# Kernel optimization log

Hardware: AMD Instinct MI355X
Metric: run time of the kernel (lower is better)

## Reference

```python
import jax, jax.numpy as jnp
import numpy as np

B, H, Wd, C = 8, 64, 64, 128
KH, KW = 3, 3
N = KH * KW  # kernel_n
F = 256


def _grid_offset(h, w, kh, kw):
    """Replicates the TensorLayer grid construction exactly, including the
    (2,kh,kw)->(kh*kw,2) reshape of the stacked meshgrid."""
    n = kh * kw
    initial = np.stack(np.meshgrid(np.arange(kh), np.arange(kw), indexing='ij'))  # (2,kh,kw)
    initial = initial.reshape(-1, 2).astype(np.float32)  # (n,2), faithful flattening order
    gy = np.arange(-int((kh - 1) / 2.0), h - int((kh - 1) / 2.0))
    gx = np.arange(-int((kw - 1) / 2.0), w - int((kw - 1) / 2.0))
    grid = np.stack(np.meshgrid(gy, gx, indexing='ij'), axis=-1).astype(np.float32)  # (h,w,2)
    grid = np.tile(grid[:, :, None, :], (1, 1, n, 1))  # (h,w,n,2)
    return jnp.asarray(grid + initial[None, None, :, :])  # (h,w,n,2)


def setup_inputs() -> dict:
    key = jax.random.key(0)
    k1, k2, k3 = jax.random.split(key, 3)
    x = jax.random.normal(k1, (B, H, Wd, C), dtype=jnp.float32)
    offsets = jax.random.normal(k2, (B, H, Wd, 2 * N), dtype=jnp.float32)
    W = jax.random.normal(k3, (N, C, F), dtype=jnp.float32) * 0.02  # truncated_normal(0.02) analogue
    b = jnp.zeros((F,), dtype=jnp.float32)
    return {"x": x, "offsets": offsets, "W": W, "b": b}


def reference(x, offsets, W, b):
    h, w = x.shape[1], x.shape[2]
    grid = _grid_offset(h, w, KH, KW)  # (h,w,n,2)
    coords = grid[None] + offsets.reshape(x.shape[0], h, w, N, 2)  # (b,h,w,n,2)
    cy = jnp.clip(coords[..., 0], 0.0, jnp.float32(h - 1))
    cx = jnp.clip(coords[..., 1], 0.0, jnp.float32(w - 1))
    y0 = jnp.floor(cy).astype(jnp.int32)
    y1 = jnp.ceil(cy).astype(jnp.int32)
    x0 = jnp.floor(cx).astype(jnp.int32)
    x1 = jnp.ceil(cx).astype(jnp.int32)

    bidx = jnp.arange(x.shape[0])[:, None, None, None]

    def gather(yy, xx):
        return x[bidx, yy, xx]  # (b,h,w,n,c)

    v_lt = gather(y0, x0)
    v_rb = gather(y1, x1)
    v_lb = gather(y0, x1)  # (lt_y, rb_x) as in original
    v_rt = gather(y1, x0)  # (rb_y, lt_x) as in original

    fy = (cy - y0.astype(cy.dtype))[..., None]
    fx = (cx - x0.astype(cx.dtype))[..., None]
    vals_t = v_lt + (v_rt - v_lt) * fy
    vals_b = v_lb + (v_rb - v_lb) * fy
    mapped = vals_t + (vals_b - vals_t) * fx  # (b,h,w,n,c)

    # conv3d with kernel [1,1,n,c,f] + VALID == contraction over (n,c)
    out = jnp.einsum('bhwnc,ncf->bhwf', mapped, W) + b
    return out
```

## Files before the change

kernel.cpp:

```cpp
#include <hip/hip_runtime.h>

#define HH 64
#define WW 64
#define CC 128
#define FF 256
#define NTAP 9
#define KD 1152
#define MTOT 32768
#define XELEMS (8 * HH * WW * CC)
#define XCVT_BLOCKS (XELEMS / (256 * 8))
#define WT_BLOCKS 144

typedef __attribute__((ext_vector_type(8))) short bf16x8;
typedef __attribute__((ext_vector_type(4))) float floatx4;

__device__ __constant__ int c_iy[9] = {0,0,1,2,2,1,0,2,1};
__device__ __constant__ int c_ix[9] = {0,1,1,2,0,2,1,0,2};

__device__ inline unsigned short f2bf(float v) {
  union { float f; unsigned u; } c; c.f = v;
  unsigned r = (c.u + 0x7FFFu + ((c.u >> 16) & 1u)) >> 16;
  return (unsigned short)r;
}
__device__ inline float bflo(unsigned u) {
  union { unsigned u; float f; } c; c.u = u << 16; return c.f;
}
__device__ inline float bfhi(unsigned u) {
  union { unsigned u; float f; } c; c.u = u & 0xFFFF0000u; return c.f;
}

__global__ void prep_kernel(const float* __restrict__ X, const float* __restrict__ W,
                            unsigned short* __restrict__ Xb, unsigned short* __restrict__ Wt) {
  const int blk = blockIdx.x;
  if (blk < XCVT_BLOCKS) {
    const int t = blk * 256 + threadIdx.x;
    const float4* src = (const float4*)(X + (size_t)t * 8);
    float4 a = src[0], b2 = src[1];
    bf16x8 o;
    o[0] = (short)f2bf(a.x);  o[1] = (short)f2bf(a.y);
    o[2] = (short)f2bf(a.z);  o[3] = (short)f2bf(a.w);
    o[4] = (short)f2bf(b2.x); o[5] = (short)f2bf(b2.y);
    o[6] = (short)f2bf(b2.z); o[7] = (short)f2bf(b2.w);
    *(bf16x8*)(Xb + (size_t)t * 8) = o;
  } else {
    const int t = (blk - XCVT_BLOCKS) * 256 + threadIdx.x;
    const int f = t & 255;
    const int k0 = (t >> 8) * 8;
    unsigned short o[8];
#pragma unroll
    for (int i2 = 0; i2 < 8; ++i2)
      o[i2] = f2bf(W[(size_t)(k0 + i2) * FF + f]);
    *(uint4*)(Wt + (size_t)f * KD + k0) = *(uint4*)o;
  }
}

__global__ __launch_bounds__(256, 4) void interp_kernel(
    const unsigned short* __restrict__ Xb, const float* __restrict__ Off,
    unsigned short* __restrict__ Mp)
{
  const int blk = blockIdx.x;
  const int b   = blk & 7;
  const int pg  = blk >> 3;
  const int tid = threadIdx.x;
  const int g   = tid >> 4;
  const int c   = tid & 15;
  const int pos_local = pg * 16 + g;
  const int y = pos_local >> 6;
  const int x = pos_local & 63;

  const unsigned short* xb = Xb + (size_t)b * (HH * WW * CC);
  const float* offp = Off + ((size_t)(b * HH + y) * WW + x) * (2 * NTAP);
  unsigned short* dstrow = Mp + (size_t)(b * 4096 + pos_local) * KD + c * 8;

#pragma unroll
  for (int n = 0; n < NTAP; ++n) {
    float2 off2 = *(const float2*)(offp + 2 * n);
    float cy = (float)(y - 1 + c_iy[n]) + off2.x;
    float cx = (float)(x - 1 + c_ix[n]) + off2.y;
    cy = fminf(fmaxf(cy, 0.f), 63.f);
    cx = fminf(fmaxf(cx, 0.f), 63.f);
    float fy0 = floorf(cy), fy1 = ceilf(cy);
    float fx0 = floorf(cx), fx1 = ceilf(cx);
    int y0 = (int)fy0, y1 = (int)fy1, x0 = (int)fx0, x1 = (int)fx1;
    float fy = cy - fy0;
    float fx = cx - fx0;

    const uint4 q00 = *(const uint4*)(xb + (y0 * WW + x0) * CC + c * 8);
    const uint4 q10 = *(const uint4*)(xb + (y1 * WW + x0) * CC + c * 8);
    const uint4 q01 = *(const uint4*)(xb + (y0 * WW + x1) * CC + c * 8);
    const uint4 q11 = *(const uint4*)(xb + (y1 * WW + x1) * CC + c * 8);

    const unsigned u00[4] = {q00.x, q00.y, q00.z, q00.w};
    const unsigned u10[4] = {q10.x, q10.y, q10.z, q10.w};
    const unsigned u01[4] = {q01.x, q01.y, q01.z, q01.w};
    const unsigned u11[4] = {q11.x, q11.y, q11.z, q11.w};

    unsigned outw[4];
#pragma unroll
    for (int j = 0; j < 4; ++j) {
      float v00 = bflo(u00[j]), v10 = bflo(u10[j]), v01 = bflo(u01[j]), v11 = bflo(u11[j]);
      float tx = v00 + (v10 - v00) * fy;
      float tb = v01 + (v11 - v01) * fy;
      unsigned short rlo = f2bf(tx + (tb - tx) * fx);
      v00 = bfhi(u00[j]); v10 = bfhi(u10[j]); v01 = bfhi(u01[j]); v11 = bfhi(u11[j]);
      tx = v00 + (v10 - v00) * fy;
      tb = v01 + (v11 - v01) * fy;
      unsigned short rhi = f2bf(tx + (tb - tx) * fx);
      outw[j] = (unsigned)rlo | ((unsigned)rhi << 16);
    }
    *(uint4*)(dstrow + n * CC) = make_uint4(outw[0], outw[1], outw[2], outw[3]);
  }
}

__global__ __launch_bounds__(256, 4) void gemm_kernel(
    const unsigned short* __restrict__ Mp, const unsigned short* __restrict__ Wt,
    const float* __restrict__ bias, float* __restrict__ Out)
{
  __shared__ unsigned short smA[64 * 64];
  __shared__ unsigned short smB[128 * 64];

  const int blk = blockIdx.x;
  const int b   = blk & 7;
  const int q   = blk >> 3;
  const int fb  = q & 1;
  const int i   = q >> 1;
  const int m0  = b * 4096 + i * 64;
  const int f0  = fb * 128;
  const int tid = threadIdx.x;
  const int wave = tid >> 6, lane = tid & 63;
  const int wm = (wave & 1) * 32;
  const int wf = (wave >> 1) * 64;
  const int arow = lane & 15, aq = lane >> 4;
  const int srow = tid >> 3;
  const int sch  = tid & 7;

  floatx4 acc[2][4];
#pragma unroll
  for (int mt = 0; mt < 2; ++mt)
#pragma unroll
    for (int ft = 0; ft < 4; ++ft)
      acc[mt][ft] = (floatx4){0.f, 0.f, 0.f, 0.f};

#define STAGE(KT)                                                                    \
  {                                                                                  \
    _Pragma("unroll")                                                                \
    for (int p = 0; p < 2; ++p) {                                                    \
      int row = p * 32 + srow;                                                       \
      int chp = sch ^ (row & 7);                                                     \
      const unsigned short* gp = Mp + (size_t)(m0 + row) * KD + (KT) * 64 + chp * 8; \
      unsigned short* l = (unsigned short*)&smA[row * 64 + sch * 8];                 \
      __builtin_amdgcn_global_load_lds(                                              \
          (const __attribute__((address_space(1))) unsigned int*)gp,                 \
          (__attribute__((address_space(3))) unsigned int*)l, 16, 0, 0);             \
    }                                                                                \
    _Pragma("unroll")                                                                \
    for (int p = 0; p < 4; ++p) {                                                    \
      int row = p * 32 + srow;                                                       \
      int chp = sch ^ (row & 7);                                                     \
      const unsigned short* gp = Wt + (size_t)(f0 + row) * KD + (KT) * 64 + chp * 8; \
      unsigned short* l = (unsigned short*)&smB[row * 64 + sch * 8];                 \
      __builtin_amdgcn_global_load_lds(                                              \
          (const __attribute__((address_space(1))) unsigned int*)gp,                 \
          (__attribute__((address_space(3))) unsigned int*)l, 16, 0, 0);             \
    }                                                                                \
  }

  STAGE(0)
  __syncthreads();

  for (int kt = 0; kt < 18; ++kt) {
#pragma unroll
    for (int ks = 0; ks < 2; ++ks) {
      bf16x8 afr[2], bfr[4];
      const int slot = (((ks * 4 + aq) ^ (arow & 7)) * 8);
#pragma unroll
      for (int mt = 0; mt < 2; ++mt)
        afr[mt] = *(const bf16x8*)&smA[(wm + mt * 16 + arow) * 64 + slot];
#pragma unroll
      for (int ft = 0; ft < 4; ++ft)
        bfr[ft] = *(const bf16x8*)&smB[(wf + ft * 16 + arow) * 64 + slot];
#pragma unroll
      for (int mt = 0; mt < 2; ++mt)
#pragma unroll
        for (int ft = 0; ft < 4; ++ft)
          acc[mt][ft] = __builtin_amdgcn_mfma_f32_16x16x32_bf16(afr[mt], bfr[ft], acc[mt][ft], 0, 0, 0);
    }
    __syncthreads();
    if (kt + 1 < 18) STAGE(kt + 1)
    __syncthreads();
  }
#undef STAGE

  float bv[4];
#pragma unroll
  for (int ft = 0; ft < 4; ++ft)
    bv[ft] = bias[f0 + wf + ft * 16 + arow];
#pragma unroll
  for (int mt = 0; mt < 2; ++mt) {
#pragma unroll
    for (int ft = 0; ft < 4; ++ft) {
      const int f = f0 + wf + ft * 16 + arow;
#pragma unroll
      for (int r = 0; r < 4; ++r) {
        const int m = m0 + wm + mt * 16 + aq * 4 + r;
        Out[(size_t)m * FF + f] = acc[mt][ft][r] + bv[ft];
      }
    }
  }
}

extern "C" void kernel_launch(void* const* d_in, const int* in_sizes, int n_in,
                              void* d_out, int out_size, void* d_ws, size_t ws_size,
                              hipStream_t stream) {
  const float* X    = (const float*)d_in[0];
  const float* Off  = (const float*)d_in[1];
  const float* W    = (const float*)d_in[2];
  const float* bias = (const float*)d_in[3];
  float* Out = (float*)d_out;

  unsigned short* Wt = (unsigned short*)d_ws;
  unsigned short* Mp = Wt + (size_t)FF * KD;
  unsigned short* Xb = Mp + (size_t)MTOT * KD;

  prep_kernel<<<XCVT_BLOCKS + WT_BLOCKS, 256, 0, stream>>>(X, W, Xb, Wt);
  interp_kernel<<<2048, 256, 0, stream>>>(Xb, Off, Mp);
  gemm_kernel<<<1024, 256, 0, stream>>>(Mp, Wt, bias, Out);
}
```

Before: 129.6 us.

## Fuse bilinear sampling into GEMM kernel, generating A tiles in shared memory

Merges the interpolation and GEMM kernels into one. Each block samples its 64 positions for the current K-tile straight into LDS and prefetches the next tile's gathers while the MFMAs run. This drops the roughly 75MB bf16 intermediate matrix written and re-read through global memory, plus one launch. Each block now covers all 256 filters with a 64x256 tile, so the grid shrinks to 512 blocks at 2 blocks per CU. That raises register pressure, and the K-loop barriers can expose the gather latency.

```diff
diff --git a/kernel.cpp b/kernel.cpp
--- a/kernel.cpp
+++ b/kernel.cpp
@@ -6,16 +6,12 @@
 #define FF 256
 #define NTAP 9
 #define KD 1152
-#define MTOT 32768
 #define XELEMS (8 * HH * WW * CC)
 #define XCVT_BLOCKS (XELEMS / (256 * 8))
 #define WT_BLOCKS 144
 
 typedef __attribute__((ext_vector_type(8))) short bf16x8;
 typedef __attribute__((ext_vector_type(4))) float floatx4;
-
-__device__ __constant__ int c_iy[9] = {0,0,1,2,2,1,0,2,1};
-__device__ __constant__ int c_ix[9] = {0,1,1,2,0,2,1,0,2};
 
 __device__ inline unsigned short f2bf(float v) {
   union { float f; unsigned u; } c; c.f = v;
@@ -27,6 +23,44 @@
 }
 __device__ inline float bfhi(unsigned u) {
   union { unsigned u; float f; } c; c.u = u & 0xFFFF0000u; return c.f;
+}
+
+__device__ inline unsigned lerp_word(unsigned u00, unsigned u10, unsigned u01, unsigned u11,
+                                     float fy, float fx) {
+  float v00 = bflo(u00), v10 = bflo(u10), v01 = bflo(u01), v11 = bflo(u11);
+  float tx = v00 + (v10 - v00) * fy;
+  float tb = v01 + (v11 - v01) * fy;
+  unsigned short rlo = f2bf(tx + (tb - tx) * fx);
+  v00 = bfhi(u00); v10 = bfhi(u10); v01 = bfhi(u01); v11 = bfhi(u11);
+  tx = v00 + (v10 - v00) * fy;
+  tb = v01 + (v11 - v01) * fy;
+  unsigned short rhi = f2bf(tx + (tb - tx) * fx);
+  return (unsigned)rlo | ((unsigned)rhi << 16);
+}
+
+#define IY_PACK 0x18690
+#define IX_PACK 0x21894
+
+struct ITap { int b00, b10, b01, b11; float fy, fx; };
+
+__device__ inline ITap interp_setup(const float* __restrict__ offp, int i, int p, int nx) {
+  const int n = nx >> 1;
+  const float2 o2 = *(const float2*)(offp + 2 * n);
+  float cy = (float)(i - 1 + ((IY_PACK >> (2 * n)) & 3)) + o2.x;
+  float cx = (float)(p - 1 + ((IX_PACK >> (2 * n)) & 3)) + o2.y;
+  cy = fminf(fmaxf(cy, 0.f), 63.f);
+  cx = fminf(fmaxf(cx, 0.f), 63.f);
+  const float fy0 = floorf(cy), fx0 = floorf(cx);
+  const int y0 = (int)fy0, y1 = (int)ceilf(cy);
+  const int x0 = (int)fx0, x1 = (int)ceilf(cx);
+  ITap t;
+  t.b00 = (y0 * WW + x0) * CC;
+  t.b10 = (y1 * WW + x0) * CC;
+  t.b01 = (y0 * WW + x1) * CC;
+  t.b11 = (y1 * WW + x1) * CC;
+  t.fy = cy - fy0;
+  t.fx = cx - fx0;
+  return t;
 }
 
 __global__ void prep_kernel(const float* __restrict__ X, const float* __restrict__ W,
@@ -54,110 +88,42 @@
   }
 }
 
-__global__ __launch_bounds__(256, 4) void interp_kernel(
+__global__ __launch_bounds__(256, 2) void fused_kernel(
     const unsigned short* __restrict__ Xb, const float* __restrict__ Off,
-    unsigned short* __restrict__ Mp)
+    const unsigned short* __restrict__ Wt, const float* __restrict__ bias,
+    float* __restrict__ Out)
 {
+  __shared__ unsigned short smA[64 * 64];
+  __shared__ unsigned short smB[256 * 64];
+
   const int blk = blockIdx.x;
   const int b   = blk & 7;
-  const int pg  = blk >> 3;
-  const int tid = threadIdx.x;
-  const int g   = tid >> 4;
-  const int c   = tid & 15;
-  const int pos_local = pg * 16 + g;
-  const int y = pos_local >> 6;
-  const int x = pos_local & 63;
-
-  const unsigned short* xb = Xb + (size_t)b * (HH * WW * CC);
-  const float* offp = Off + ((size_t)(b * HH + y) * WW + x) * (2 * NTAP);
-  unsigned short* dstrow = Mp + (size_t)(b * 4096 + pos_local) * KD + c * 8;
-
-#pragma unroll
-  for (int n = 0; n < NTAP; ++n) {
-    float2 off2 = *(const float2*)(offp + 2 * n);
-    float cy = (float)(y - 1 + c_iy[n]) + off2.x;
-    float cx = (float)(x - 1 + c_ix[n]) + off2.y;
-    cy = fminf(fmaxf(cy, 0.f), 63.f);
-    cx = fminf(fmaxf(cx, 0.f), 63.f);
-    float fy0 = floorf(cy), fy1 = ceilf(cy);
-    float fx0 = floorf(cx), fx1 = ceilf(cx);
-    int y0 = (int)fy0, y1 = (int)fy1, x0 = (int)fx0, x1 = (int)fx1;
-    float fy = cy - fy0;
-    float fx = cx - fx0;
-
-    const uint4 q00 = *(const uint4*)(xb + (y0 * WW + x0) * CC + c * 8);
-    const uint4 q10 = *(const uint4*)(xb + (y1 * WW + x0) * CC + c * 8);
-    const uint4 q01 = *(const uint4*)(xb + (y0 * WW + x1) * CC + c * 8);
-    const uint4 q11 = *(const uint4*)(xb + (y1 * WW + x1) * CC + c * 8);
-
-    const unsigned u00[4] = {q00.x, q00.y, q00.z, q00.w};
-    const unsigned u10[4] = {q10.x, q10.y, q10.z, q10.w};
-    const unsigned u01[4] = {q01.x, q01.y, q01.z, q01.w};
-    const unsigned u11[4] = {q11.x, q11.y, q11.z, q11.w};
-
-    unsigned outw[4];
-#pragma unroll
-    for (int j = 0; j < 4; ++j) {
-      float v00 = bflo(u00[j]), v10 = bflo(u10[j]), v01 = bflo(u01[j]), v11 = bflo(u11[j]);
-      float tx = v00 + (v10 - v00) * fy;
-      float tb = v01 + (v11 - v01) * fy;
-      unsigned short rlo = f2bf(tx + (tb - tx) * fx);
-      v00 = bfhi(u00[j]); v10 = bfhi(u10[j]); v01 = bfhi(u01[j]); v11 = bfhi(u11[j]);
-      tx = v00 + (v10 - v00) * fy;
-      tb = v01 + (v11 - v01) * fy;
-      unsigned short rhi = f2bf(tx + (tb - tx) * fx);
-      outw[j] = (unsigned)rlo | ((unsigned)rhi << 16);
-    }
-    *(uint4*)(dstrow + n * CC) = make_uint4(outw[0], outw[1], outw[2], outw[3]);
-  }
-}
-
-__global__ __launch_bounds__(256, 4) void gemm_kernel(
-    const unsigned short* __restrict__ Mp, const unsigned short* __restrict__ Wt,
-    const float* __restrict__ bias, float* __restrict__ Out)
-{
-  __shared__ unsigned short smA[64 * 64];
-  __shared__ unsigned short smB[128 * 64];
-
-  const int blk = blockIdx.x;
-  const int b   = blk & 7;
-  const int q   = blk >> 3;
-  const int fb  = q & 1;
-  const int i   = q >> 1;
-  const int m0  = b * 4096 + i * 64;
-  const int f0  = fb * 128;
+  const int i   = blk >> 3;
+  const int m0  = (b * 64 + i) * 64;
   const int tid = threadIdx.x;
   const int wave = tid >> 6, lane = tid & 63;
-  const int wm = (wave & 1) * 32;
-  const int wf = (wave >> 1) * 64;
+  const int wf   = wave * 64;
   const int arow = lane & 15, aq = lane >> 4;
-  const int srow = tid >> 3;
-  const int sch  = tid & 7;
-
-  floatx4 acc[2][4];
-#pragma unroll
-  for (int mt = 0; mt < 2; ++mt)
+  const int srow = tid >> 3, sch = tid & 7;
+  const int p = tid >> 2, c0 = tid & 3;
+
+  const unsigned short* xb = Xb + (size_t)b * (HH * WW * CC);
+  const float* offp = Off + ((size_t)(b * HH + i) * WW + p) * (2 * NTAP);
+
+  floatx4 acc[4][4];
+#pragma unroll
+  for (int mt = 0; mt < 4; ++mt)
 #pragma unroll
     for (int ft = 0; ft < 4; ++ft)
       acc[mt][ft] = (floatx4){0.f, 0.f, 0.f, 0.f};
 
-#define STAGE(KT)                                                                    \
+#define STAGE_B(KT)                                                                  \
   {                                                                                  \
     _Pragma("unroll")                                                                \
-    for (int p = 0; p < 2; ++p) {                                                    \
-      int row = p * 32 + srow;                                                       \
-      int chp = sch ^ (row & 7);                                                     \
-      const unsigned short* gp = Mp + (size_t)(m0 + row) * KD + (KT) * 64 + chp * 8; \
-      unsigned short* l = (unsigned short*)&smA[row * 64 + sch * 8];                 \
-      __builtin_amdgcn_global_load_lds(                                              \
-          (const __attribute__((address_space(1))) unsigned int*)gp,                 \
-          (__attribute__((address_space(3))) unsigned int*)l, 16, 0, 0);             \
-    }                                                                                \
-    _Pragma("unroll")                                                                \
-    for (int p = 0; p < 4; ++p) {                                                    \
-      int row = p * 32 + srow;                                                       \
-      int chp = sch ^ (row & 7);                                                     \
-      const unsigned short* gp = Wt + (size_t)(f0 + row) * KD + (KT) * 64 + chp * 8; \
+    for (int q2 = 0; q2 < 8; ++q2) {                                                 \
+      const int row = q2 * 32 + srow;                                                \
+      const int chp = sch ^ (row & 7);                                               \
+      const unsigned short* gp = Wt + (size_t)row * KD + (KT) * 64 + chp * 8;        \
       unsigned short* l = (unsigned short*)&smB[row * 64 + sch * 8];                 \
       __builtin_amdgcn_global_load_lds(                                              \
           (const __attribute__((address_space(1))) unsigned int*)gp,                 \
@@ -165,44 +131,94 @@
     }                                                                                \
   }
 
-  STAGE(0)
+  {
+    ITap t = interp_setup(offp, i, p, 0);
+#pragma unroll
+    for (int cc = 0; cc < 2; ++cc) {
+      const int c = c0 + cc * 4;
+      const int ch = c << 3;
+      uint4 q00 = *(const uint4*)(xb + t.b00 + ch);
+      uint4 q10 = *(const uint4*)(xb + t.b10 + ch);
+      uint4 q01 = *(const uint4*)(xb + t.b01 + ch);
+      uint4 q11 = *(const uint4*)(xb + t.b11 + ch);
+      unsigned ow0 = lerp_word(q00.x, q10.x, q01.x, q11.x, t.fy, t.fx);
+      unsigned ow1 = lerp_word(q00.y, q10.y, q01.y, q11.y, t.fy, t.fx);
+      unsigned ow2 = lerp_word(q00.z, q10.z, q01.z, q11.z, t.fy, t.fx);
+      unsigned ow3 = lerp_word(q00.w, q10.w, q01.w, q11.w, t.fy, t.fx);
+      *(uint4*)&smA[p * 64 + ((c ^ (p & 7)) << 3)] = make_uint4(ow0, ow1, ow2, ow3);
+    }
+    STAGE_B(0)
+  }
   __syncthreads();
 
   for (int kt = 0; kt < 18; ++kt) {
+    bf16x8 afr[2][4], bfr[2][4];
 #pragma unroll
     for (int ks = 0; ks < 2; ++ks) {
-      bf16x8 afr[2], bfr[4];
-      const int slot = (((ks * 4 + aq) ^ (arow & 7)) * 8);
-#pragma unroll
-      for (int mt = 0; mt < 2; ++mt)
-        afr[mt] = *(const bf16x8*)&smA[(wm + mt * 16 + arow) * 64 + slot];
+      const int slot = (((ks * 4 + aq) ^ (arow & 7)) << 3);
+#pragma unroll
+      for (int mt = 0; mt < 4; ++mt)
+        afr[ks][mt] = *(const bf16x8*)&smA[(mt * 16 + arow) * 64 + slot];
 #pragma unroll
       for (int ft = 0; ft < 4; ++ft)
-        bfr[ft] = *(const bf16x8*)&smB[(wf + ft * 16 + arow) * 64 + slot];
-#pragma unroll
-      for (int mt = 0; mt < 2; ++mt)
+        bfr[ks][ft] = *(const bf16x8*)&smB[(wf + ft * 16 + arow) * 64 + slot];
+    }
+    __syncthreads();
+
+    const int nx = kt + 1;
+    ITap t;
+    uint4 g[2][4];
+    if (nx < 18) {
+      t = interp_setup(offp, i, p, nx);
+      const int gc = (nx & 1) << 3;
+#pragma unroll
+      for (int cc = 0; cc < 2; ++cc) {
+        const int ch = (gc + c0 + cc * 4) << 3;
+        g[cc][0] = *(const uint4*)(xb + t.b00 + ch);
+        g[cc][1] = *(const uint4*)(xb + t.b10 + ch);
+        g[cc][2] = *(const uint4*)(xb + t.b01 + ch);
+        g[cc][3] = *(const uint4*)(xb + t.b11 + ch);
+      }
+      STAGE_B(nx)
+    }
+
+#pragma unroll
+    for (int ks = 0; ks < 2; ++ks)
+#pragma unroll
+      for (int mt = 0; mt < 4; ++mt)
 #pragma unroll
         for (int ft = 0; ft < 4; ++ft)
-          acc[mt][ft] = __builtin_amdgcn_mfma_f32_16x16x32_bf16(afr[mt], bfr[ft], acc[mt][ft], 0, 0, 0);
+          acc[mt][ft] = __builtin_amdgcn_mfma_f32_16x16x32_bf16(
+              afr[ks][mt], bfr[ks][ft], acc[mt][ft], 0, 0, 0);
+
+    if (nx < 18) {
+#pragma unroll
+      for (int cc = 0; cc < 2; ++cc) {
+        const int c = c0 + cc * 4;
+        uint4 q00 = g[cc][0], q10 = g[cc][1], q01 = g[cc][2], q11 = g[cc][3];
+        unsigned ow0 = lerp_word(q00.x, q10.x, q01.x, q11.x, t.fy, t.fx);
+        unsigned ow1 = lerp_word(q00.y, q10.y, q01.y, q11.y, t.fy, t.fx);
+        unsigned ow2 = lerp_word(q00.z, q10.z, q01.z, q11.z, t.fy, t.fx);
+        unsigned ow3 = lerp_word(q00.w, q10.w, q01.w, q11.w, t.fy, t.fx);
+        *(uint4*)&smA[p * 64 + ((c ^ (p & 7)) << 3)] = make_uint4(ow0, ow1, ow2, ow3);
+      }
     }
     __syncthreads();
-    if (kt + 1 < 18) STAGE(kt + 1)
-    __syncthreads();
-  }
-#undef STAGE
+  }
+#undef STAGE_B
 
   float bv[4];
 #pragma unroll
   for (int ft = 0; ft < 4; ++ft)
-    bv[ft] = bias[f0 + wf + ft * 16 + arow];
-#pragma unroll
-  for (int mt = 0; mt < 2; ++mt) {
+    bv[ft] = bias[wf + ft * 16 + arow];
+#pragma unroll
+  for (int mt = 0; mt < 4; ++mt) {
 #pragma unroll
     for (int ft = 0; ft < 4; ++ft) {
-      const int f = f0 + wf + ft * 16 + arow;
+      const int f = wf + ft * 16 + arow;
 #pragma unroll
       for (int r = 0; r < 4; ++r) {
-        const int m = m0 + wm + mt * 16 + aq * 4 + r;
+        const int m = m0 + mt * 16 + aq * 4 + r;
         Out[(size_t)m * FF + f] = acc[mt][ft][r] + bv[ft];
       }
     }
@@ -219,10 +235,8 @@
   float* Out = (float*)d_out;
 
   unsigned short* Wt = (unsigned short*)d_ws;
-  unsigned short* Mp = Wt + (size_t)FF * KD;
-  unsigned short* Xb = Mp + (size_t)MTOT * KD;
+  unsigned short* Xb = Wt + (size_t)FF * KD;
 
   prep_kernel<<<XCVT_BLOCKS + WT_BLOCKS, 256, 0, stream>>>(X, W, Xb, Wt);
-  interp_kernel<<<2048, 256, 0, stream>>>(Xb, Off, Mp);
-  gemm_kernel<<<1024, 256, 0, stream>>>(Mp, Wt, bias, Out);
-}
+  fused_kernel<<<512, 256, 0, stream>>>(Xb, Off, Wt, bias, Out);
+}
```

New measurement: 120.1 us. -7.4%, faster.
